# Kernel tuning notes

Measured on AMD Instinct MI355X. Metric: run time of the kernel, lower is better.

## Reference

```python
import jax, jax.numpy as jnp
import numpy as np

BETA = 0.25  # commitment loss weight


def setup_inputs() -> dict:
    key = jax.random.key(0)
    ks = jax.random.split(key, 6)
    B, H, W, C = 16, 64, 64, 128
    x = jax.random.normal(ks[0], (B, H, W, C), dtype=jnp.float32)
    # dictionaries: sizes 2^6 .. 2^9 (from num_embeddings=[64,512]),
    # keras RandomUniform default init in (-0.05, 0.05)
    dicts = {}
    for i, n_emb in enumerate([64, 128, 256, 512]):
        dicts[f"dict{i}"] = jax.random.uniform(
            ks[i + 1], (C, n_emb), dtype=jnp.float32, minval=-0.05, maxval=0.05)
    vq_alpha = jnp.asarray(1.0, dtype=jnp.float32)
    vq_gamma = jnp.full((4,), 0.25, dtype=jnp.float32)  # 1/num_dictionaries
    return {"x": x, **dicts, "vq_alpha": vq_alpha, "vq_gamma": vq_gamma}


def _vq_pass(flat, D):
    # flat: [N, C], D: [C, K]. Squared-euclidean distances then argmin.
    dist = (jnp.sum(flat * flat, axis=1, keepdims=True)
            + jnp.sum(D * D, axis=0)[None, :]
            - 2.0 * (flat @ D))  # [N, K]
    idx = jnp.argmin(dist, axis=1)  # [N]
    # one_hot @ D.T  ==  gather rows of D.T
    return jnp.take(D.T, idx, axis=0)  # [N, C]


def reference(x, dict0, dict1, dict2, dict3, vq_alpha, vq_gamma):
    dicts = [dict0, dict1, dict2, dict3]
    C = x.shape[-1]
    flat = x.reshape(-1, C)  # [N, C]
    weighted_q = jnp.zeros_like(x)
    dictionary_loss = jnp.asarray(0.0, x.dtype)
    commitment_loss = jnp.asarray(0.0, x.dtype)
    for i, D in enumerate(dicts):
        q = (vq_alpha * _vq_pass(flat, D)).reshape(x.shape)
        weighted_q = weighted_q + vq_gamma[i] * q
        dictionary_loss += vq_gamma[i] * jnp.mean(
            jnp.square(jax.lax.stop_gradient(x) - q))
        commitment_loss += vq_gamma[i] * jnp.mean(
            jnp.square(x - jax.lax.stop_gradient(q)))
    loss = dictionary_loss + BETA * commitment_loss
    # straight-through estimator
    out = x + jax.lax.stop_gradient(weighted_q - x)
    return out, loss
```

## Files before the change

kernel.cpp:

```cpp
#include <hip/hip_runtime.h>

#define CDIM 128
#define NC   8388608

typedef __attribute__((ext_vector_type(8)))  short bf8v;
typedef __attribute__((ext_vector_type(16))) float f32x16;


__device__ __forceinline__ void bsplit(float v, short& h, short& lo) {
  unsigned u = __float_as_uint(v);
  unsigned hb = (u + 0x7fffu + ((u >> 16) & 1u)) >> 16;
  float hf = __uint_as_float(hb << 16);
  float lf = v - hf;
  unsigned u2 = __float_as_uint(lf);
  unsigned lb = (u2 + 0x7fffu + ((u2 >> 16) & 1u)) >> 16;
  h = (short)hb; lo = (short)lb;
}

__global__ void vq_prep(const float* __restrict__ D0, const float* __restrict__ D1,
                        const float* __restrict__ D2, const float* __restrict__ D3,
                        float* __restrict__ nrm, float* __restrict__ DT) {
  int g = blockIdx.x * 256 + threadIdx.x;
  if (g >= 960) return;
  const float* D; int K, k; float* T;
  if (g < 64)       { D = D0; K = 64;  k = g;       T = DT; }
  else if (g < 192) { D = D1; K = 128; k = g - 64;  T = DT + 8192; }
  else if (g < 448) { D = D2; K = 256; k = g - 192; T = DT + 24576; }
  else              { D = D3; K = 512; k = g - 448; T = DT + 57344; }
  float s = 0.f;
  for (int c = 0; c < 128; ++c) { float v = D[c*K+k]; s = fmaf(v,v,s); T[k*128+c] = v; }
  nrm[g] = s;
}

__global__ void vq_pack(const float* __restrict__ D0, const float* __restrict__ D1,
                        const float* __restrict__ D2, const float* __restrict__ D3,
                        bf8v* __restrict__ Bph, bf8v* __restrict__ Bpl) {
  int g = blockIdx.x * 256 + threadIdx.x;
  int T = g >> 9, c = (g >> 6) & 7, l = g & 63;
  int col = T * 32 + (l & 31);
  int k0 = c * 16 + (l >> 5) * 8;
  const float* D; int K, cb;
  if (col < 64)       { D = D0; K = 64;  cb = col; }
  else if (col < 192) { D = D1; K = 128; cb = col - 64; }
  else if (col < 448) { D = D2; K = 256; cb = col - 192; }
  else                { D = D3; K = 512; cb = col - 448; }
  short h0,h1,h2,h3,h4,h5,h6,h7, q0,q1,q2,q3,q4,q5,q6,q7;
  bsplit(D[(k0+0)*K + cb], h0, q0);
  bsplit(D[(k0+1)*K + cb], h1, q1);
  bsplit(D[(k0+2)*K + cb], h2, q2);
  bsplit(D[(k0+3)*K + cb], h3, q3);
  bsplit(D[(k0+4)*K + cb], h4, q4);
  bsplit(D[(k0+5)*K + cb], h5, q5);
  bsplit(D[(k0+6)*K + cb], h6, q6);
  bsplit(D[(k0+7)*K + cb], h7, q7);
  Bph[g] = (bf8v){h0,h1,h2,h3,h4,h5,h6,h7};
  Bpl[g] = (bf8v){q0,q1,q2,q3,q4,q5,q6,q7};
}

#define MK8(U0, U1, HD, LD) { \
  short h0,h1,h2,h3,h4,h5,h6,h7, q0,q1,q2,q3,q4,q5,q6,q7; \
  bsplit(U0.x,h0,q0); bsplit(U0.y,h1,q1); bsplit(U0.z,h2,q2); bsplit(U0.w,h3,q3); \
  bsplit(U1.x,h4,q4); bsplit(U1.y,h5,q5); bsplit(U1.z,h6,q6); bsplit(U1.w,h7,q7); \
  HD = (bf8v){h0,h1,h2,h3,h4,h5,h6,h7}; \
  LD = (bf8v){q0,q1,q2,q3,q4,q5,q6,q7}; }

#define MFMA32(AC, AF, BF) AC = __builtin_amdgcn_mfma_f32_32x32x16_bf16((AF), (BF), (AC), 0, 0, 0)

#define PF_T(TT) { \
  const bf8v* __restrict__ gh = Bph + (TT) * 512; \
  const bf8v* __restrict__ gl = Bpl + (TT) * 512; \
  pf0 = gh[t]; pf1 = gh[256 + t]; pf2 = gl[t]; pf3 = gl[256 + t]; }

#define STORE_T(BF) { \
  BL[BF][t] = pf0; BL[BF][256 + t] = pf1; BL[BF][512 + t] = pf2; BL[BF][768 + t] = pf3; }

#define COMPUTE_T(T, BF) { \
  f32x16 ae = zero16, ao = zero16; \
  _Pragma("unroll") \
  for (int cp = 0; cp < 4; ++cp) { \
    const int ce = 2*cp, co = 2*cp+1; \
    bf8v bhe = BL[BF][ce*64 + l]; bf8v bho = BL[BF][co*64 + l]; \
    bf8v ble = BL[BF][512 + ce*64 + l]; bf8v blo = BL[BF][512 + co*64 + l]; \
    MFMA32(ae, Ah[ce], bhe); MFMA32(ao, Ah[co], bho); \
    MFMA32(ae, Al[ce], bhe); MFMA32(ao, Al[co], bho); \
    MFMA32(ae, Ah[ce], ble); MFMA32(ao, Ah[co], blo); \
  } \
  f32x16 sv = ae + ao; \
  const float nv = nrm_g[(T)*32 + (l & 31)]; \
  const int colT = (T)*32 + (l & 31); \
  _Pragma("unroll") \
  for (int r = 0; r < 16; ++r) { \
    float c0 = fmaf(-2.f, sv[r], nv); \
    if (c0 < bc[r]) { bc[r] = c0; bk[r] = colT; } } }

#define ROUND_T(T) { \
  if ((T) < 29) { \
    STORE_T(((T) + 1) & 1); \
    const int TN = ((T) + 2 <= 29) ? (T) + 2 : 29; \
    PF_T(TN); \
  } \
  COMPUTE_T(T, (T) & 1) \
  __syncthreads(); }

#define FLUSH1(DICTID, BASE) { \
  _Pragma("unroll") \
  for (int r = 0; r < 16; ++r) { \
    float b0 = bc[r]; int K0 = bk[r]; \
    _Pragma("unroll") \
    for (int m = 1; m <= 16; m <<= 1) { \
      float pb = __shfl_xor(b0, m); int pk = __shfl_xor(K0, m); \
      if (pb < b0 || (pb == b0 && pk < K0)) { b0 = pb; K0 = pk; } } \
    if ((l & 31) == 0) { \
      const int ro = (r & 3) + 8 * (r >> 2) + 4 * hl; \
      keys[((rowbase + ro) << 2) | (DICTID)] = K0 - (BASE); } \
    bc[r] = 1e30f; bk[r] = 0; } }

__global__ __launch_bounds__(256, 2) void vq_mfma(
    const float* __restrict__ x,
    const bf8v* __restrict__ Bph, const bf8v* __restrict__ Bpl,
    const float* __restrict__ nrm_g, int* __restrict__ keys)
{
  __shared__ bf8v BL[2][1024];

  const int t = threadIdx.x;
  const int w = t >> 6, l = t & 63;
  const int hl = l >> 5;
  const int rowbase = blockIdx.x * 128 + w * 32;

  bf8v Ah[8], Al[8];
  {
    const float* __restrict__ xr = x + (size_t)(rowbase + (l & 31)) * CDIM + hl * 8;
    #pragma unroll
    for (int c = 0; c < 8; ++c) {
      float4 u0 = *(const float4*)(xr + c * 16);
      float4 u1 = *(const float4*)(xr + c * 16 + 4);
      MK8(u0, u1, Ah[c], Al[c])
    }
  }

  f32x16 zero16;
  #pragma unroll
  for (int i = 0; i < 16; ++i) zero16[i] = 0.f;

  float bc[16]; int bk[16];
  #pragma unroll
  for (int r = 0; r < 16; ++r) { bc[r] = 1e30f; bk[r] = 0; }

  bf8v pf0, pf1, pf2, pf3;
  PF_T(0)
  STORE_T(0)
  PF_T(1)
  __syncthreads();

  ROUND_T(0) ROUND_T(1)
  FLUSH1(0, 0)
  for (int T = 2; T < 6; ++T) ROUND_T(T)
  FLUSH1(1, 64)
  for (int T = 6; T < 14; ++T) ROUND_T(T)
  FLUSH1(2, 192)
  for (int T = 14; T < 30; ++T) ROUND_T(T)
  FLUSH1(3, 448)
}

__global__ __launch_bounds__(256, 8) void vq_merge(
    const float* __restrict__ x, const float* __restrict__ DT,
    const int* __restrict__ keys,
    const float* __restrict__ alpha_p, const float* __restrict__ gamma_p,
    float* __restrict__ out, float* __restrict__ partials)
{
  __shared__ int kk[32][4];
  __shared__ float wr[4];
  const int t = threadIdx.x;
  const int row0 = blockIdx.x * 32;
  if (t < 128) {
    int r = t >> 2, d = t & 3;
    kk[r][d] = keys[((row0 + r) << 2) | d];
  }
  __syncthreads();
  const float a = alpha_p[0];
  const float g0 = gamma_p[0], g1 = gamma_p[1], g2 = gamma_p[2], g3 = gamma_p[3];
  float lc = 0.f;
  #pragma unroll
  for (int j = 0; j < 4; ++j) {
    const int f = j * 256 + t;
    const int r = f >> 5, c4 = (f & 31) * 4;
    const size_t off = (size_t)(row0 + r) * CDIM + c4;
    const float4 xv = *(const float4*)(x + off);
    const float4 d0 = *(const float4*)(DT +         kk[r][0] * 128 + c4);
    const float4 d1 = *(const float4*)(DT +  8192 + kk[r][1] * 128 + c4);
    const float4 d2 = *(const float4*)(DT + 24576 + kk[r][2] * 128 + c4);
    const float4 d3 = *(const float4*)(DT + 57344 + kk[r][3] * 128 + c4);
    float4 o;
    o.x = a * (g0*d0.x + g1*d1.x + g2*d2.x + g3*d3.x);
    o.y = a * (g0*d0.y + g1*d1.y + g2*d2.y + g3*d3.y);
    o.z = a * (g0*d0.z + g1*d1.z + g2*d2.z + g3*d3.z);
    o.w = a * (g0*d0.w + g1*d1.w + g2*d2.w + g3*d3.w);
    *(float4*)(out + off) = o;
    float e0, e1, e2, e3;
    e0 = fmaf(-a, d0.x, xv.x); e1 = fmaf(-a, d1.x, xv.x);
    e2 = fmaf(-a, d2.x, xv.x); e3 = fmaf(-a, d3.x, xv.x);
    lc += g0*e0*e0 + g1*e1*e1 + g2*e2*e2 + g3*e3*e3;
    e0 = fmaf(-a, d0.y, xv.y); e1 = fmaf(-a, d1.y, xv.y);
    e2 = fmaf(-a, d2.y, xv.y); e3 = fmaf(-a, d3.y, xv.y);
    lc += g0*e0*e0 + g1*e1*e1 + g2*e2*e2 + g3*e3*e3;
    e0 = fmaf(-a, d0.z, xv.z); e1 = fmaf(-a, d1.z, xv.z);
    e2 = fmaf(-a, d2.z, xv.z); e3 = fmaf(-a, d3.z, xv.z);
    lc += g0*e0*e0 + g1*e1*e1 + g2*e2*e2 + g3*e3*e3;
    e0 = fmaf(-a, d0.w, xv.w); e1 = fmaf(-a, d1.w, xv.w);
    e2 = fmaf(-a, d2.w, xv.w); e3 = fmaf(-a, d3.w, xv.w);
    lc += g0*e0*e0 + g1*e1*e1 + g2*e2*e2 + g3*e3*e3;
  }
  #pragma unroll
  for (int off2 = 32; off2 > 0; off2 >>= 1) lc += __shfl_down(lc, off2);
  if ((t & 63) == 0) wr[t >> 6] = lc;
  __syncthreads();
  if (t == 0) partials[blockIdx.x] = wr[0] + wr[1] + wr[2] + wr[3];
}

__global__ void vq_loss(const float* __restrict__ partials, float* __restrict__ lossp) {
  __shared__ float wr[4];
  const int t = threadIdx.x;
  float v = 0.f;
  #pragma unroll
  for (int i = 0; i < 8; ++i) v += partials[i * 256 + t];
  #pragma unroll
  for (int off = 32; off > 0; off >>= 1) v += __shfl_down(v, off);
  if ((t & 63) == 0) wr[t >> 6] = v;
  __syncthreads();
  if (t == 0) lossp[0] = (wr[0] + wr[1] + wr[2] + wr[3]) * (1.25f / 8388608.f);
}

extern "C" void kernel_launch(void* const* d_in, const int* in_sizes, int n_in,
                              void* d_out, int out_size, void* d_ws, size_t ws_size,
                              hipStream_t stream) {
  const float* x  = (const float*)d_in[0];
  const float* D0 = (const float*)d_in[1];
  const float* D1 = (const float*)d_in[2];
  const float* D2 = (const float*)d_in[3];
  const float* D3 = (const float*)d_in[4];
  const float* alpha = (const float*)d_in[5];
  const float* gamma = (const float*)d_in[6];
  float* out = (float*)d_out;

  float* ws  = (float*)d_ws;
  float* nrm = ws;
  float* DT  = ws + 1024;
  bf8v*  Bph = (bf8v*)(ws + 123904);
  bf8v*  Bpl = (bf8v*)(ws + 185344);
  int*  keys = (int*)(ws + 246784);
  float* partials = ws + 508928;

  vq_prep<<<4, 256, 0, stream>>>(D0, D1, D2, D3, nrm, DT);
  vq_pack<<<60, 256, 0, stream>>>(D0, D1, D2, D3, Bph, Bpl);
  vq_mfma<<<512, 256, 0, stream>>>(x, Bph, Bpl, nrm, keys);
  vq_merge<<<2048, 256, 0, stream>>>(x, DT, keys, alpha, gamma, out, partials);
  vq_loss<<<1, 256, 0, stream>>>(partials, out + NC);
}
```

Baseline: 100.0 us.

## Fuse merge and loss into MFMA kernel, compute loss algebraically from distances

Folds the gather/merge stage into the MFMA argmin kernel: keys stay in shared memory, and the output rows are written straight from the dictionary transpose without re-reading x. The loss is rebuilt from each row's best distance, its codeword norm and ||x||^2 instead of elementwise error sums. The prep and pack kernels are merged into one launch. This removes the keys round trip, one full read of x and two kernel launches. In exchange, loss precision now rests on the split-bf16 distance values, and the argmin kernel takes on the output writes.

```diff
diff --git a/kernel.cpp b/kernel.cpp
--- a/kernel.cpp
+++ b/kernel.cpp
@@ -19,42 +19,42 @@
 
 __global__ void vq_prep(const float* __restrict__ D0, const float* __restrict__ D1,
                         const float* __restrict__ D2, const float* __restrict__ D3,
-                        float* __restrict__ nrm, float* __restrict__ DT) {
-  int g = blockIdx.x * 256 + threadIdx.x;
-  if (g >= 960) return;
-  const float* D; int K, k; float* T;
-  if (g < 64)       { D = D0; K = 64;  k = g;       T = DT; }
-  else if (g < 192) { D = D1; K = 128; k = g - 64;  T = DT + 8192; }
-  else if (g < 448) { D = D2; K = 256; k = g - 192; T = DT + 24576; }
-  else              { D = D3; K = 512; k = g - 448; T = DT + 57344; }
-  float s = 0.f;
-  for (int c = 0; c < 128; ++c) { float v = D[c*K+k]; s = fmaf(v,v,s); T[k*128+c] = v; }
-  nrm[g] = s;
-}
-
-__global__ void vq_pack(const float* __restrict__ D0, const float* __restrict__ D1,
-                        const float* __restrict__ D2, const float* __restrict__ D3,
+                        float* __restrict__ nrm, float* __restrict__ DT,
                         bf8v* __restrict__ Bph, bf8v* __restrict__ Bpl) {
-  int g = blockIdx.x * 256 + threadIdx.x;
-  int T = g >> 9, c = (g >> 6) & 7, l = g & 63;
-  int col = T * 32 + (l & 31);
-  int k0 = c * 16 + (l >> 5) * 8;
-  const float* D; int K, cb;
-  if (col < 64)       { D = D0; K = 64;  cb = col; }
-  else if (col < 192) { D = D1; K = 128; cb = col - 64; }
-  else if (col < 448) { D = D2; K = 256; cb = col - 192; }
-  else                { D = D3; K = 512; cb = col - 448; }
-  short h0,h1,h2,h3,h4,h5,h6,h7, q0,q1,q2,q3,q4,q5,q6,q7;
-  bsplit(D[(k0+0)*K + cb], h0, q0);
-  bsplit(D[(k0+1)*K + cb], h1, q1);
-  bsplit(D[(k0+2)*K + cb], h2, q2);
-  bsplit(D[(k0+3)*K + cb], h3, q3);
-  bsplit(D[(k0+4)*K + cb], h4, q4);
-  bsplit(D[(k0+5)*K + cb], h5, q5);
-  bsplit(D[(k0+6)*K + cb], h6, q6);
-  bsplit(D[(k0+7)*K + cb], h7, q7);
-  Bph[g] = (bf8v){h0,h1,h2,h3,h4,h5,h6,h7};
-  Bpl[g] = (bf8v){q0,q1,q2,q3,q4,q5,q6,q7};
+  const int b = blockIdx.x;
+  if (b < 60) {
+    int g = b * 256 + threadIdx.x;
+    int T = g >> 9, c = (g >> 6) & 7, l = g & 63;
+    int col = T * 32 + (l & 31);
+    int k0 = c * 16 + (l >> 5) * 8;
+    const float* D; int K, cb;
+    if (col < 64)       { D = D0; K = 64;  cb = col; }
+    else if (col < 192) { D = D1; K = 128; cb = col - 64; }
+    else if (col < 448) { D = D2; K = 256; cb = col - 192; }
+    else                { D = D3; K = 512; cb = col - 448; }
+    short h0,h1,h2,h3,h4,h5,h6,h7, q0,q1,q2,q3,q4,q5,q6,q7;
+    bsplit(D[(k0+0)*K + cb], h0, q0);
+    bsplit(D[(k0+1)*K + cb], h1, q1);
+    bsplit(D[(k0+2)*K + cb], h2, q2);
+    bsplit(D[(k0+3)*K + cb], h3, q3);
+    bsplit(D[(k0+4)*K + cb], h4, q4);
+    bsplit(D[(k0+5)*K + cb], h5, q5);
+    bsplit(D[(k0+6)*K + cb], h6, q6);
+    bsplit(D[(k0+7)*K + cb], h7, q7);
+    Bph[g] = (bf8v){h0,h1,h2,h3,h4,h5,h6,h7};
+    Bpl[g] = (bf8v){q0,q1,q2,q3,q4,q5,q6,q7};
+  } else {
+    int g = (b - 60) * 256 + threadIdx.x;
+    if (g >= 960) return;
+    const float* D; int K, k; float* T;
+    if (g < 64)       { D = D0; K = 64;  k = g;       T = DT; }
+    else if (g < 192) { D = D1; K = 128; k = g - 64;  T = DT + 8192; }
+    else if (g < 448) { D = D2; K = 256; k = g - 192; T = DT + 24576; }
+    else              { D = D3; K = 512; k = g - 448; T = DT + 57344; }
+    float s = 0.f;
+    for (int c = 0; c < 128; ++c) { float v = D[c*K+k]; s = fmaf(v,v,s); T[k*128+c] = v; }
+    nrm[g] = s;
+  }
 }
 
 #define MK8(U0, U1, HD, LD) { \
@@ -102,7 +102,7 @@
   COMPUTE_T(T, (T) & 1) \
   __syncthreads(); }
 
-#define FLUSH1(DICTID, BASE) { \
+#define FLUSH1(DICTID, BASE, GAM) { \
   _Pragma("unroll") \
   for (int r = 0; r < 16; ++r) { \
     float b0 = bc[r]; int K0 = bk[r]; \
@@ -112,31 +112,51 @@
       if (pb < b0 || (pb == b0 && pk < K0)) { b0 = pb; K0 = pk; } } \
     if ((l & 31) == 0) { \
       const int ro = (r & 3) + 8 * (r >> 2) + 4 * hl; \
-      keys[((rowbase + ro) << 2) | (DICTID)] = K0 - (BASE); } \
+      keysL[DICTID][w * 32 + ro] = K0 - (BASE); \
+      const float nst = nrm_g[K0]; \
+       \
+      lossacc = fmaf((GAM) * a, fmaf(am1, nst, b0), lossacc); } \
     bc[r] = 1e30f; bk[r] = 0; } }
 
 __global__ __launch_bounds__(256, 2) void vq_mfma(
     const float* __restrict__ x,
     const bf8v* __restrict__ Bph, const bf8v* __restrict__ Bpl,
-    const float* __restrict__ nrm_g, int* __restrict__ keys)
+    const float* __restrict__ nrm_g, const float* __restrict__ DT,
+    const float* __restrict__ alpha_p, const float* __restrict__ gamma_p,
+    float* __restrict__ out, float* __restrict__ partials)
 {
-  __shared__ bf8v BL[2][1024];
+  __shared__ bf8v  BL[2][1024];
+  __shared__ int   keysL[4][128];
+  __shared__ float lossW[4];
 
   const int t = threadIdx.x;
   const int w = t >> 6, l = t & 63;
   const int hl = l >> 5;
   const int rowbase = blockIdx.x * 128 + w * 32;
 
+  const float a  = alpha_p[0];
+  const float am1 = a - 1.f;
+  const float g0 = gamma_p[0], g1 = gamma_p[1], g2 = gamma_p[2], g3 = gamma_p[3];
+  const float gsum = g0 + g1 + g2 + g3;
+
   bf8v Ah[8], Al[8];
+  float xsqh = 0.f;
   {
     const float* __restrict__ xr = x + (size_t)(rowbase + (l & 31)) * CDIM + hl * 8;
     #pragma unroll
     for (int c = 0; c < 8; ++c) {
       float4 u0 = *(const float4*)(xr + c * 16);
       float4 u1 = *(const float4*)(xr + c * 16 + 4);
+      xsqh = fmaf(u0.x,u0.x, xsqh); xsqh = fmaf(u0.y,u0.y, xsqh);
+      xsqh = fmaf(u0.z,u0.z, xsqh); xsqh = fmaf(u0.w,u0.w, xsqh);
+      xsqh = fmaf(u1.x,u1.x, xsqh); xsqh = fmaf(u1.y,u1.y, xsqh);
+      xsqh = fmaf(u1.z,u1.z, xsqh); xsqh = fmaf(u1.w,u1.w, xsqh);
       MK8(u0, u1, Ah[c], Al[c])
     }
   }
+  float xs_ = xsqh;
+  #pragma unroll
+  for (int m = 1; m <= 32; m <<= 1) xs_ += __shfl_xor(xs_, m);
 
   f32x16 zero16;
   #pragma unroll
@@ -145,6 +165,7 @@
   float bc[16]; int bk[16];
   #pragma unroll
   for (int r = 0; r < 16; ++r) { bc[r] = 1e30f; bk[r] = 0; }
+  float lossacc = 0.f;
 
   bf8v pf0, pf1, pf2, pf3;
   PF_T(0)
@@ -153,76 +174,45 @@
   __syncthreads();
 
   ROUND_T(0) ROUND_T(1)
-  FLUSH1(0, 0)
+  FLUSH1(0, 0, g0)
   for (int T = 2; T < 6; ++T) ROUND_T(T)
-  FLUSH1(1, 64)
+  FLUSH1(1, 64, g1)
   for (int T = 6; T < 14; ++T) ROUND_T(T)
-  FLUSH1(2, 192)
+  FLUSH1(2, 192, g2)
   for (int T = 14; T < 30; ++T) ROUND_T(T)
-  FLUSH1(3, 448)
-}
-
-__global__ __launch_bounds__(256, 8) void vq_merge(
-    const float* __restrict__ x, const float* __restrict__ DT,
-    const int* __restrict__ keys,
-    const float* __restrict__ alpha_p, const float* __restrict__ gamma_p,
-    float* __restrict__ out, float* __restrict__ partials)
-{
-  __shared__ int kk[32][4];
-  __shared__ float wr[4];
-  const int t = threadIdx.x;
-  const int row0 = blockIdx.x * 32;
-  if (t < 128) {
-    int r = t >> 2, d = t & 3;
-    kk[r][d] = keys[((row0 + r) << 2) | d];
+  FLUSH1(3, 448, g3)
+
+  {
+    float wl = lossacc + __shfl_xor(lossacc, 32);
+    if (l == 0) lossW[w] = fmaf(gsum, xs_, wl);
   }
   __syncthreads();
-  const float a = alpha_p[0];
-  const float g0 = gamma_p[0], g1 = gamma_p[1], g2 = gamma_p[2], g3 = gamma_p[3];
-  float lc = 0.f;
-  #pragma unroll
-  for (int j = 0; j < 4; ++j) {
+  if (t == 0) partials[blockIdx.x] = lossW[0] + lossW[1] + lossW[2] + lossW[3];
+
+  #pragma unroll 4
+  for (int j = 0; j < 16; ++j) {
     const int f = j * 256 + t;
     const int r = f >> 5, c4 = (f & 31) * 4;
-    const size_t off = (size_t)(row0 + r) * CDIM + c4;
-    const float4 xv = *(const float4*)(x + off);
-    const float4 d0 = *(const float4*)(DT +         kk[r][0] * 128 + c4);
-    const float4 d1 = *(const float4*)(DT +  8192 + kk[r][1] * 128 + c4);
-    const float4 d2 = *(const float4*)(DT + 24576 + kk[r][2] * 128 + c4);
-    const float4 d3 = *(const float4*)(DT + 57344 + kk[r][3] * 128 + c4);
+    const int kk0 = keysL[0][r], kk1 = keysL[1][r];
+    const int kk2 = keysL[2][r], kk3 = keysL[3][r];
+    const size_t off = (size_t)(blockIdx.x * 128 + r) * CDIM + c4;
+    const float4 d0 = *(const float4*)(DT +         kk0 * 128 + c4);
+    const float4 d1 = *(const float4*)(DT +  8192 + kk1 * 128 + c4);
+    const float4 d2 = *(const float4*)(DT + 24576 + kk2 * 128 + c4);
+    const float4 d3 = *(const float4*)(DT + 57344 + kk3 * 128 + c4);
     float4 o;
     o.x = a * (g0*d0.x + g1*d1.x + g2*d2.x + g3*d3.x);
     o.y = a * (g0*d0.y + g1*d1.y + g2*d2.y + g3*d3.y);
     o.z = a * (g0*d0.z + g1*d1.z + g2*d2.z + g3*d3.z);
     o.w = a * (g0*d0.w + g1*d1.w + g2*d2.w + g3*d3.w);
     *(float4*)(out + off) = o;
-    float e0, e1, e2, e3;
-    e0 = fmaf(-a, d0.x, xv.x); e1 = fmaf(-a, d1.x, xv.x);
-    e2 = fmaf(-a, d2.x, xv.x); e3 = fmaf(-a, d3.x, xv.x);
-    lc += g0*e0*e0 + g1*e1*e1 + g2*e2*e2 + g3*e3*e3;
-    e0 = fmaf(-a, d0.y, xv.y); e1 = fmaf(-a, d1.y, xv.y);
-    e2 = fmaf(-a, d2.y, xv.y); e3 = fmaf(-a, d3.y, xv.y);
-    lc += g0*e0*e0 + g1*e1*e1 + g2*e2*e2 + g3*e3*e3;
-    e0 = fmaf(-a, d0.z, xv.z); e1 = fmaf(-a, d1.z, xv.z);
-    e2 = fmaf(-a, d2.z, xv.z); e3 = fmaf(-a, d3.z, xv.z);
-    lc += g0*e0*e0 + g1*e1*e1 + g2*e2*e2 + g3*e3*e3;
-    e0 = fmaf(-a, d0.w, xv.w); e1 = fmaf(-a, d1.w, xv.w);
-    e2 = fmaf(-a, d2.w, xv.w); e3 = fmaf(-a, d3.w, xv.w);
-    lc += g0*e0*e0 + g1*e1*e1 + g2*e2*e2 + g3*e3*e3;
-  }
-  #pragma unroll
-  for (int off2 = 32; off2 > 0; off2 >>= 1) lc += __shfl_down(lc, off2);
-  if ((t & 63) == 0) wr[t >> 6] = lc;
-  __syncthreads();
-  if (t == 0) partials[blockIdx.x] = wr[0] + wr[1] + wr[2] + wr[3];
+  }
 }
 
 __global__ void vq_loss(const float* __restrict__ partials, float* __restrict__ lossp) {
   __shared__ float wr[4];
   const int t = threadIdx.x;
-  float v = 0.f;
-  #pragma unroll
-  for (int i = 0; i < 8; ++i) v += partials[i * 256 + t];
+  float v = partials[t] + partials[t + 256];
   #pragma unroll
   for (int off = 32; off > 0; off >>= 1) v += __shfl_down(v, off);
   if ((t & 63) == 0) wr[t >> 6] = v;
@@ -247,12 +237,9 @@
   float* DT  = ws + 1024;
   bf8v*  Bph = (bf8v*)(ws + 123904);
   bf8v*  Bpl = (bf8v*)(ws + 185344);
-  int*  keys = (int*)(ws + 246784);
-  float* partials = ws + 508928;
-
-  vq_prep<<<4, 256, 0, stream>>>(D0, D1, D2, D3, nrm, DT);
-  vq_pack<<<60, 256, 0, stream>>>(D0, D1, D2, D3, Bph, Bpl);
-  vq_mfma<<<512, 256, 0, stream>>>(x, Bph, Bpl, nrm, keys);
-  vq_merge<<<2048, 256, 0, stream>>>(x, DT, keys, alpha, gamma, out, partials);
+  float* partials = ws + 246784;
+
+  vq_prep<<<64, 256, 0, stream>>>(D0, D1, D2, D3, nrm, DT, Bph, Bpl);
+  vq_mfma<<<512, 256, 0, stream>>>(x, Bph, Bpl, nrm, DT, alpha, gamma, out, partials);
   vq_loss<<<1, 256, 0, stream>>>(partials, out + NC);
 }
```

Result: slower. 104.2 us (+4.2%).
